# Kernel tuning notes

Measured on AMD Instinct MI355X. Metric: run time of the kernel, lower is better.

Reference implementation:

```python
import jax, jax.numpy as jnp
import numpy as np

NUM_ENT = 100000
NUM_REL = 400
EMB = 100          # emb_dim
OUT = 200          # 2*emb_dim (GCN out channels / ConvE embedding)
E = 500000         # num edges (even: first half 'in', second half 'out')
B = 512            # batch of triples
BN_EPS = 1e-5


def ccorr(a, b):
    # circular correlation: irfft(conj(rfft(a)) * rfft(b))
    fa = jnp.fft.rfft(a, axis=-1)
    fb = jnp.fft.rfft(b, axis=-1)
    return jnp.fft.irfft(jnp.conj(fa) * fb, n=a.shape[-1], axis=-1).astype(a.dtype)


def bn(x, axes):
    # training-mode batchnorm with default affine (gamma=1, beta=0)
    m = jnp.mean(x, axis=axes, keepdims=True)
    v = jnp.var(x, axis=axes, keepdims=True)
    return (x - m) * jax.lax.rsqrt(v + BN_EPS)


def setup_inputs() -> dict:
    key = jax.random.key(0)
    ks = jax.random.split(key, 18)
    s = 0.1
    return {
        'ent_emb': jax.random.normal(ks[0], (NUM_ENT, EMB), jnp.float32) * s,
        'rel_emb': jax.random.normal(ks[1], (NUM_REL, EMB), jnp.float32) * s,
        'in_w': jax.random.normal(ks[2], (EMB, OUT), jnp.float32) * s,
        'out_w': jax.random.normal(ks[3], (EMB, OUT), jnp.float32) * s,
        'loop_w': jax.random.normal(ks[4], (EMB, OUT), jnp.float32) * s,
        'w_rel': jax.random.normal(ks[5], (EMB, OUT), jnp.float32) * s,
        'loop_rel': jax.random.normal(ks[6], (1, EMB), jnp.float32) * s,
        'gcn_bias': jnp.zeros((OUT,), jnp.float32),
        'edge_norm': jax.random.uniform(ks[7], (E,), jnp.float32),
        'conv_w': jax.random.normal(ks[8], (200, 1, 7, 7), jnp.float32) * 0.05,
        'fc_w': jax.random.normal(ks[9], (OUT, 39200), jnp.float32) * 0.01,
        'fc_b': jnp.zeros((OUT,), jnp.float32),
        'b_ent': jnp.zeros((NUM_ENT,), jnp.float32),
        'edge_src': jax.random.randint(ks[10], (E,), 0, NUM_ENT, jnp.int32),
        'edge_dst': jax.random.randint(ks[11], (E,), 0, NUM_ENT, jnp.int32),
        'edge_type': jax.random.randint(ks[12], (E,), 0, NUM_REL, jnp.int32),
        'head': jax.random.randint(ks[13], (B,), 0, NUM_ENT, jnp.int32),
        'rela': jax.random.randint(ks[14], (B,), 0, NUM_REL, jnp.int32),
    }


def reference(ent_emb, rel_emb, in_w, out_w, loop_w, w_rel, loop_rel,
              gcn_bias, edge_norm, conv_w, fc_w, fc_b, b_ent,
              edge_src, edge_dst, edge_type, head, rela):
    # ---- CompGCNCov layer (opn='corr', act=tanh, dropout off / eval) ----
    edge_data = ccorr(ent_emb[edge_src], rel_emb[edge_type])      # [E, EMB]
    half = edge_data.shape[0] // 2
    msg = jnp.concatenate([edge_data[:half] @ in_w,
                           edge_data[half:] @ out_w], axis=0)     # [E, OUT]
    msg = msg * edge_norm[:, None]
    agg = jax.ops.segment_sum(msg, edge_dst, num_segments=ent_emb.shape[0]) / 3.0
    loop = ccorr(ent_emb, jnp.broadcast_to(loop_rel, ent_emb.shape)) @ loop_w / 3.0
    x = agg + loop + gcn_bias
    x = jnp.tanh(bn(x, (0,)))                                     # [NUM_ENT, OUT]
    r = rel_emb @ w_rel                                           # [NUM_REL, OUT]

    # ---- ConvE decoder ----
    h = x[head]                                                   # [B, OUT]
    q = r[rela]                                                   # [B, OUT]
    stack = jnp.concatenate([h[:, None, :], q[:, None, :]], axis=1)
    stack = stack.reshape(-1, 1, 20, 20)                          # [B,1,20,20]
    z = bn(stack, (0, 2, 3))
    z = jax.lax.conv_general_dilated(z, conv_w, (1, 1), 'VALID',
                                     dimension_numbers=('NCHW', 'OIHW', 'NCHW'))
    z = jax.nn.relu(bn(z, (0, 2, 3)))                             # [B,200,14,14]
    z = z.reshape(z.shape[0], -1) @ fc_w.T + fc_b                 # [B, OUT]
    z = jax.nn.relu(bn(z, (0,)))
    score = jax.nn.sigmoid(z @ x.T + b_ent)                       # [B, NUM_ENT]
    return score
```

## Files before the change

### kernel.cpp

```cpp
#include <hip/hip_runtime.h>

#define NENT  100000
#define NREL  400
#define EMB   100
#define NF    51
#define FCMP  102
#define OUTC  200
#define NEDGE 500000
#define HALFE 250000
#define BATCH 512
#define POSN  196
#define FCK   39200
#define BN_EPS 1e-5f
#define CAP   16
#define KSPLIT 175
#define NCOL8  208
#define FCOUT  106496

static constexpr size_t OFF_FA     = 0;
static constexpr size_t OFF_XH     = 0;
static constexpr size_t OFF_ACCIN  = 10200000;
static constexpr size_t OFF_Z1H    = 10200000;
static constexpr size_t OFF_ACCOUT = 20400000;
static constexpr size_t OFF_FCWH   = 20400000;
static constexpr size_t OFF_XBUF   = 30600000;
static constexpr size_t OFF_FB     = 50600000;
static constexpr size_t OFF_FL     = 50640800;
static constexpr size_t OFF_BIGBT  = 50640928;
static constexpr size_t OFF_R      = 50675872;
static constexpr size_t OFF_IMG    = 50755872;
static constexpr size_t OFF_DFTH   = 50755872;
static constexpr size_t OFF_ZH     = 50755872;
static constexpr size_t OFF_DFTC   = 50960672;
static constexpr size_t OFF_DFTS   = 50965772;
static constexpr size_t OFF_Z      = 50970872;
static constexpr size_t OFF_COLSUM = OFF_Z + 102400;
static constexpr size_t OFF_COLSS  = OFF_COLSUM + 200;
static constexpr size_t OFF_BN1    = OFF_COLSS + 200;
static constexpr size_t OFF_CHSUM  = OFF_BN1 + 8;
static constexpr size_t OFF_CHSS   = OFF_CHSUM + 200;
static constexpr size_t WS_END     = OFF_CHSS + 200;

#define NBUCK 200000
static constexpr size_t BK_CNT   = 0;
static constexpr size_t BK_OVFN  = 200000;
static constexpr size_t BK_OVF   = 200004;
static constexpr size_t BK_SLOT  = 700008;

typedef __attribute__((ext_vector_type(8))) _Float16 f16x8;
typedef __attribute__((ext_vector_type(4))) _Float16 f16x4;
typedef __attribute__((ext_vector_type(4))) float f32x4;

__device__ inline unsigned int pkc(float re, float im) {
  union { _Float16 h[2]; unsigned int u; } c;
  c.h[0] = (_Float16)re; c.h[1] = (_Float16)im;
  return c.u;
}
__device__ inline float2 unpk(unsigned int w) {
  union { unsigned int u; _Float16 h[2]; } c; c.u = w;
  return make_float2((float)c.h[0], (float)c.h[1]);
}
__device__ inline float sigf(float v) {
  return __builtin_amdgcn_rcpf(1.0f + __expf(-v));
}

__global__ void k_tables(float* __restrict__ ws) {
  int i = blockIdx.x * 256 + threadIdx.x;
  if (i >= EMB * NF) return;
  int j = i / NF, f = i - j * NF;
  int m = (j * f) % EMB;
  float ang = (float)m * 0.06283185307179586f;
  ws[OFF_DFTC + i] = cosf(ang);
  ws[OFF_DFTS + i] = sinf(ang);
}

__global__ void k_dfth(_Float16* __restrict__ DT) {
  int i = blockIdx.x * 256 + threadIdx.x;
  if (i >= 112 * 128) return;
  int c = i >> 7, k = i & 127;
  float v = 0.f;
  if (c < FCMP && k < EMB) {
    int f = c >> 1;
    int m = (k * f) % EMB;
    float ang = (float)m * 0.06283185307179586f;
    v = (c & 1) ? -sinf(ang) : cosf(ang);
  }
  DT[i] = (_Float16)v;
}

__global__ void __launch_bounds__(256) k_rfft_mfma(const float* __restrict__ A,
                                                   const _Float16* __restrict__ DT,
                                                   _Float16* __restrict__ Fa) {
  int t = threadIdx.x;
  int w = t >> 6, l = t & 63;
  int lr = l & 15, kg = l >> 4;
  size_t row0 = (size_t)blockIdx.x * 128 + w * 32;
  f32x4 acc[2][7];
  #pragma unroll
  for (int i = 0; i < 2; ++i)
    #pragma unroll
    for (int j = 0; j < 7; ++j) acc[i][j] = (f32x4){0.f, 0.f, 0.f, 0.f};

  #pragma unroll
  for (int st = 0; st < 4; ++st) {
    int koff = st * 32 + kg * 8;
    f16x8 a[2];
    #pragma unroll
    for (int i = 0; i < 2; ++i) {
      size_t row = row0 + i * 16 + lr;
      if (row >= NENT) row = NENT - 1;
      f16x8 h;
      if (st < 3) {
        const float* p = A + row * EMB + koff;
        float4 p0 = *(const float4*)p;
        float4 p1 = *(const float4*)(p + 4);
        h[0] = (_Float16)p0.x; h[1] = (_Float16)p0.y; h[2] = (_Float16)p0.z; h[3] = (_Float16)p0.w;
        h[4] = (_Float16)p1.x; h[5] = (_Float16)p1.y; h[6] = (_Float16)p1.z; h[7] = (_Float16)p1.w;
      } else if (kg == 0) {
        float4 p0 = *(const float4*)(A + row * EMB + 96);
        h[0] = (_Float16)p0.x; h[1] = (_Float16)p0.y; h[2] = (_Float16)p0.z; h[3] = (_Float16)p0.w;
        h[4] = (_Float16)0.f; h[5] = (_Float16)0.f; h[6] = (_Float16)0.f; h[7] = (_Float16)0.f;
      } else {
        h = (f16x8)0;
      }
      a[i] = h;
    }
    f16x8 b[7];
    #pragma unroll
    for (int j = 0; j < 7; ++j)
      b[j] = *(const f16x8*)(DT + (size_t)(j * 16 + lr) * 128 + koff);
    #pragma unroll
    for (int i = 0; i < 2; ++i)
      #pragma unroll
      for (int j = 0; j < 7; ++j)
        acc[i][j] = __builtin_amdgcn_mfma_f32_16x16x32_f16(a[i], b[j], acc[i][j], 0, 0, 0);
  }

  #pragma unroll
  for (int i = 0; i < 2; ++i) {
    #pragma unroll
    for (int j = 0; j < 7; ++j) {
      int col = j * 16 + lr;
      if (col < FCMP) {
        #pragma unroll
        for (int r = 0; r < 4; ++r) {
          size_t row = row0 + i * 16 + kg * 4 + r;
          if (row < NENT) Fa[row * FCMP + col] = (_Float16)acc[i][j][r];
        }
      }
    }
  }
}

__global__ void k_rfft(const float* __restrict__ src, unsigned int* __restrict__ dst,
                       const float* __restrict__ dftc, const float* __restrict__ dfts,
                       int nrows) {
  __shared__ float arow[4][EMB];
  int g = threadIdx.x >> 6;
  int lane = threadIdx.x & 63;
  int row = blockIdx.x * 4 + g;
  if (row < nrows) {
    for (int j = lane; j < EMB; j += 64) arow[g][j] = src[(size_t)row * EMB + j];
  }
  __syncthreads();
  if (row < nrows && lane < NF) {
    float re = 0.f, im = 0.f;
    for (int j = 0; j < EMB; ++j) {
      float a = arow[g][j];
      re += a * dftc[j * NF + lane];
      im -= a * dfts[j * NF + lane];
    }
    dst[(size_t)row * NF + lane] = pkc(re, im);
  }
}

__global__ void k_wtilde(const float* __restrict__ in_w, const float* __restrict__ out_w,
                         const float* __restrict__ loop_w, float* __restrict__ ws) {
  int id = blockIdx.x * 256 + threadIdx.x;
  if (id >= NF * OUTC) return;
  int f = id / OUTC, o = id - f * OUTC;
  const float* dftc = ws + OFF_DFTC;
  const float* dfts = ws + OFF_DFTS;
  float ci = 0, si = 0, co = 0, so = 0, cl = 0, sl = 0;
  for (int k = 0; k < EMB; ++k) {
    float c = dftc[k * NF + f], s = dfts[k * NF + f];
    float wi = in_w[k * OUTC + o], wo = out_w[k * OUTC + o], wl = loop_w[k * OUTC + o];
    ci += c * wi; si += s * wi;
    co += c * wo; so += s * wo;
    cl += c * wl; sl += s * wl;
  }
  bool ends = (f == 0) || (f == NF - 1);
  float mult = ends ? 1.0f : 2.0f;
  const float inv3n = 1.0f / (3.0f * (float)EMB);
  _Float16* bt = (_Float16*)(ws + OFF_BIGBT);
  size_t ro = (size_t)o * 336;
  bt[ro + 102 + 2 * f]     = (_Float16)(mult * ci * inv3n);
  bt[ro + 102 + 2 * f + 1] = (_Float16)(ends ? 0.f : (-2.0f * si * inv3n));
  bt[ro + 204 + 2 * f]     = (_Float16)(mult * co * inv3n);
  bt[ro + 204 + 2 * f + 1] = (_Float16)(ends ? 0.f : (-2.0f * so * inv3n));
  float wlre = mult * cl * inv3n;
  float wlim = ends ? 0.f : (-2.0f * sl * inv3n);
  float2 fl = unpk(((const unsigned int*)(ws + OFF_FL))[f]);
  bt[ro + 2 * f]     = (_Float16)(fl.x * wlre + fl.y * wlim);
  bt[ro + 2 * f + 1] = (_Float16)(fl.y * wlre - fl.x * wlim);
}

__global__ void k_bucket(const int* __restrict__ edst, const int* __restrict__ esrc,
                         const int* __restrict__ etyp, const float* __restrict__ enorm,
                         int* __restrict__ cnt, uint2* __restrict__ slot,
                         int* __restrict__ ovfn, int* __restrict__ ovf) {
  int e = blockIdx.x * 256 + threadIdx.x;
  if (e >= NEDGE) return;
  int b = (e < HALFE ? 0 : NENT) + edst[e];
  int pos = atomicAdd(&cnt[b], 1);
  if (pos < CAP) {
    unsigned int p = (unsigned int)esrc[e] | ((unsigned int)etyp[e] << 17);
    slot[(size_t)b * CAP + pos] = make_uint2(p, __float_as_uint(enorm[e]));
  } else {
    int oi = atomicAdd(ovfn, 1);
    if (oi < NEDGE) ovf[oi] = e;
  }
}

__global__ void __launch_bounds__(256) k_agg(const unsigned int* __restrict__ faw,
                                             const unsigned int* __restrict__ fbw,
                                             const int* __restrict__ cnt,
                                             const uint2* __restrict__ slot,
                                             float* __restrict__ accIn, float* __restrict__ accOut) {
  int g = threadIdx.x >> 6;
  int lane = threadIdx.x & 63;
  int d = blockIdx.x * 2 + (g >> 1);
  int sub = g & 1;
  int bucket = sub * NENT + d;
  int n = cnt[bucket];
  if (n > CAP) n = CAP;
  const uint2* sl = slot + (size_t)bucket * CAP;
  uint2 my = make_uint2(0u, 0u);
  if (lane < n) my = sl[lane];
  float ar = 0.f, ai = 0.f;
  for (int i = 0; i < n; i += 4) {
    #pragma unroll
    for (int u = 0; u < 4; ++u) {
      int iu = i + u;
      int ic = (iu < n) ? iu : (n - 1);
      unsigned int p = (unsigned int)__shfl((int)my.x, ic);
      float nor = __uint_as_float((unsigned int)__shfl((int)my.y, ic));
      if (iu >= n) nor = 0.f;
      int s = (int)(p & 0x1FFFFu);
      int ty = (int)(p >> 17);
      if (lane < NF) {
        float2 fa = unpk(faw[(size_t)s * NF + lane]);
        float2 fb = unpk(fbw[(size_t)ty * NF + lane]);
        ar += (fa.x * fb.x + fa.y * fb.y) * nor;
        ai += (fa.x * fb.y - fa.y * fb.x) * nor;
      }
    }
  }
  if (lane < NF) {
    float* dst = sub ? accOut : accIn;
    *(float2*)(dst + (size_t)d * FCMP + 2 * lane) = make_float2(ar, ai);
  }
}

__global__ void k_ovf(const unsigned int* __restrict__ faw, const unsigned int* __restrict__ fbw,
                      const int* __restrict__ esrc, const int* __restrict__ edst,
                      const int* __restrict__ etyp, const float* __restrict__ enorm,
                      const int* __restrict__ ovfn, const int* __restrict__ ovf,
                      float* __restrict__ accIn, float* __restrict__ accOut) {
  int sub = threadIdx.x >> 7;
  int l = threadIdx.x & 127;
  if (l >= FCMP) return;
  int n = *ovfn;
  if (n > NEDGE) n = NEDGE;
  int f = l >> 1, isim = l & 1;
  for (int j = blockIdx.x * 2 + sub; j < n; j += gridDim.x * 2) {
    int e = ovf[j];
    int s = esrc[e], d = edst[e], ty = etyp[e];
    float nor = enorm[e];
    float2 fa = unpk(faw[(size_t)s * NF + f]);
    float2 fb = unpk(fbw[(size_t)ty * NF + f]);
    float v = isim ? (fa.x * fb.y - fa.y * fb.x) : (fa.x * fb.x + fa.y * fb.y);
    float* acc = (e < HALFE) ? accIn : accOut;
    atomicAdd(acc + (size_t)d * FCMP + l, v * nor);
  }
}

__global__ void k_relmat(const float* __restrict__ rel_emb, const float* __restrict__ w_rel,
                         float* __restrict__ r) {
  int id = blockIdx.x * 256 + threadIdx.x;
  if (id >= NREL * OUTC) return;
  int rr = id / OUTC, o = id - rr * OUTC;
  float acc = 0.f;
  for (int k = 0; k < EMB; ++k) acc += rel_emb[rr * EMB + k] * w_rel[k * OUTC + o];
  r[id] = acc;
}

__global__ void __launch_bounds__(256) k_fused_x_mfma(const float* __restrict__ ws,
                                                      _Float16* __restrict__ xpre) {
  int t = threadIdx.x;
  int w = t >> 6, l = t & 63;
  int lr = l & 15, kg = l >> 4;
  size_t row0 = (size_t)blockIdx.x * 128 + w * 32;
  const _Float16* BT = (const _Float16*)(ws + OFF_BIGBT);
  const _Float16* FaH = (const _Float16*)(ws + OFF_FA);
  const float* aI = ws + OFF_ACCIN;
  const float* aO = ws + OFF_ACCOUT;
  f32x4 acc[2][13];
  #pragma unroll
  for (int i = 0; i < 2; ++i)
    #pragma unroll
    for (int j = 0; j < 13; ++j) acc[i][j] = (f32x4){0.f, 0.f, 0.f, 0.f};

  #pragma unroll
  for (int seg = 0; seg < 3; ++seg) {
    #pragma unroll
    for (int st = 0; st < 4; ++st) {
      int koff = st * 32 + kg * 8;
      f16x8 a[2];
      #pragma unroll
      for (int i = 0; i < 2; ++i) {
        size_t row = row0 + i * 16 + lr;
        f16x8 h;
        if (seg == 0) {
          h = *(const f16x8*)(FaH + row * FCMP + koff);
          if (st == 3) {
            #pragma unroll
            for (int e = 0; e < 8; ++e)
              if (koff + e >= FCMP) h[e] = (_Float16)0.f;
          }
        } else {
          const float* p = (seg == 1 ? aI : aO) + row * FCMP + koff;
          float4 p0 = *(const float4*)p;
          float4 p1 = *(const float4*)(p + 4);
          if (st < 3) {
            h[0] = (_Float16)p0.x; h[1] = (_Float16)p0.y; h[2] = (_Float16)p0.z; h[3] = (_Float16)p0.w;
            h[4] = (_Float16)p1.x; h[5] = (_Float16)p1.y; h[6] = (_Float16)p1.z; h[7] = (_Float16)p1.w;
          } else {
            float pv[8] = {p0.x, p0.y, p0.z, p0.w, p1.x, p1.y, p1.z, p1.w};
            #pragma unroll
            for (int e = 0; e < 8; ++e)
              h[e] = (koff + e < FCMP) ? (_Float16)pv[e] : (_Float16)0.f;
          }
        }
        a[i] = h;
      }
      f16x8 b[13];
      #pragma unroll
      for (int j = 0; j < 13; ++j)
        b[j] = *(const f16x8*)(BT + (size_t)(j * 16 + lr) * 336 + seg * FCMP + koff);
      #pragma unroll
      for (int i = 0; i < 2; ++i)
        #pragma unroll
        for (int j = 0; j < 13; ++j)
          acc[i][j] = __builtin_amdgcn_mfma_f32_16x16x32_f16(a[i], b[j], acc[i][j], 0, 0, 0);
    }
  }

  #pragma unroll
  for (int i = 0; i < 2; ++i) {
    #pragma unroll
    for (int j = 0; j < 13; ++j) {
      int col = j * 16 + lr;
      if (col < OUTC) {
        #pragma unroll
        for (int r = 0; r < 4; ++r) {
          size_t row = row0 + i * 16 + kg * 4 + r;
          if (row < NENT) xpre[row * OUTC + col] = (_Float16)acc[i][j][r];
        }
      }
    }
  }
}

__global__ void k_colstats(const _Float16* __restrict__ x, float* __restrict__ colsum,
                           float* __restrict__ colss) {
  int t = threadIdx.x;
  if (t >= OUTC) return;
  size_t r0 = (size_t)blockIdx.x * 500;
  float s1 = 0.f, s2 = 0.f;
  for (int i = 0; i < 500; ++i) {
    float v = (float)x[(r0 + i) * OUTC + t];
    s1 += v; s2 += v * v;
  }
  atomicAdd(colsum + t, s1);
  atomicAdd(colss + t, s2);
}

__global__ void k_bn_tanh(const _Float16* __restrict__ x, _Float16* __restrict__ xh,
                          const float* __restrict__ colsum, const float* __restrict__ colss) {
  size_t i = (size_t)blockIdx.x * 256 + threadIdx.x;
  if (i >= 5000000ull) return;
  f16x4 v = ((const f16x4*)x)[i];
  int c = (int)((i * 4) % OUTC);
  const float inv = 1.0f / (float)NENT;
  float m, q, rs;
  f16x4 h;
  m = colsum[c] * inv;     q = colss[c] * inv - m * m;     rs = rsqrtf(q + BN_EPS); h[0] = (_Float16)tanhf(((float)v[0] - m) * rs);
  m = colsum[c + 1] * inv; q = colss[c + 1] * inv - m * m; rs = rsqrtf(q + BN_EPS); h[1] = (_Float16)tanhf(((float)v[1] - m) * rs);
  m = colsum[c + 2] * inv; q = colss[c + 2] * inv - m * m; rs = rsqrtf(q + BN_EPS); h[2] = (_Float16)tanhf(((float)v[2] - m) * rs);
  m = colsum[c + 3] * inv; q = colss[c + 3] * inv - m * m; rs = rsqrtf(q + BN_EPS); h[3] = (_Float16)tanhf(((float)v[3] - m) * rs);
  *(f16x4*)(xh + i * 4) = h;
}

__global__ void k_fcw_h(const float* __restrict__ w, _Float16* __restrict__ wh) {
  size_t i = (size_t)blockIdx.x * 256 + threadIdx.x;
  if (i >= 980000ull) return;
  float4 v0 = ((const float4*)w)[i * 2];
  float4 v1 = ((const float4*)w)[i * 2 + 1];
  f16x8 h;
  h[0] = (_Float16)v0.x; h[1] = (_Float16)v0.y; h[2] = (_Float16)v0.z; h[3] = (_Float16)v0.w;
  h[4] = (_Float16)v1.x; h[5] = (_Float16)v1.y; h[6] = (_Float16)v1.z; h[7] = (_Float16)v1.w;
  ((f16x8*)wh)[i] = h;
}

__global__ void k_gather_img(const _Float16* __restrict__ xh, const float* __restrict__ r,
                             const int* __restrict__ head, const int* __restrict__ rela,
                             float* __restrict__ img, float* __restrict__ bn1) {
  int b = blockIdx.x, t = threadIdx.x;
  int h = head[b], q = rela[b];
  float s1 = 0.f, s2 = 0.f;
  for (int j = t; j < 400; j += 256) {
    float v = (j < OUTC) ? (float)xh[(size_t)h * OUTC + j] : r[(size_t)q * OUTC + (j - OUTC)];
    img[(size_t)b * 400 + j] = v;
    s1 += v; s2 += v * v;
  }
  for (int off = 32; off; off >>= 1) { s1 += __shfl_down(s1, off); s2 += __shfl_down(s2, off); }
  if ((t & 63) == 0) { atomicAdd(bn1, s1); atomicAdd(bn1 + 1, s2); }
}

__global__ void __launch_bounds__(256) k_conv(const float* __restrict__ img, const float* __restrict__ conv_w,
                                              const float* __restrict__ bn1, _Float16* __restrict__ z1,
                                              float* __restrict__ chsum, float* __restrict__ chss) {
  __shared__ float imgn[400];
  int b = blockIdx.x, t = threadIdx.x;
  float m = bn1[0] * (1.0f / 204800.0f);
  float var = bn1[1] * (1.0f / 204800.0f) - m * m;
  float rs = rsqrtf(var + BN_EPS);
  for (int j = t; j < 400; j += 256) imgn[j] = (img[(size_t)b * 400 + j] - m) * rs;
  __syncthreads();
  if (t < OUTC) {
    float w[49];
    #pragma unroll
    for (int i = 0; i < 49; ++i) w[i] = conv_w[t * 49 + i];
    float s1 = 0.f, s2 = 0.f;
    size_t base = (size_t)b * FCK + (size_t)t * POSN;
    for (int pos = 0; pos < POSN; ++pos) {
      int y = pos / 14, xx = pos - y * 14;
      float acc = 0.f;
      #pragma unroll
      for (int ky = 0; ky < 7; ++ky)
        #pragma unroll
        for (int kx = 0; kx < 7; ++kx)
          acc += imgn[(y + ky) * 20 + xx + kx] * w[ky * 7 + kx];
      z1[base + pos] = (_Float16)acc;
      s1 += acc; s2 += acc * acc;
    }
    atomicAdd(chsum + t, s1);
    atomicAdd(chss + t, s2);
  }
}

__global__ void k_bn2_relu(_Float16* __restrict__ z1, const float* __restrict__ chsum,
                           const float* __restrict__ chss) {
  size_t i = (size_t)blockIdx.x * 256 + threadIdx.x;
  if (i >= 5017600ull) return;
  f16x4 v = ((f16x4*)z1)[i];
  int c = (int)((i * 4 % FCK) / POSN);
  const float inv = 1.0f / (512.0f * 196.0f);
  float m = chsum[c] * inv;
  float var = chss[c] * inv - m * m;
  float rs = rsqrtf(var + BN_EPS);
  #pragma unroll
  for (int e = 0; e < 4; ++e)
    v[e] = (_Float16)fmaxf(((float)v[e] - m) * rs, 0.f);
  ((f16x4*)z1)[i] = v;
}

__global__ void __launch_bounds__(256) k_fc_mfma(const _Float16* __restrict__ A,
                                                 const _Float16* __restrict__ B,
                                                 float* __restrict__ partial) {
  int t = threadIdx.x;
  int w = t >> 6, l = t & 63;
  int lr = l & 15, kg = l >> 4;
  int m0 = blockIdx.y * 128 + w * 32;
  int ks = blockIdx.x;
  f32x4 acc[2][13];
  #pragma unroll
  for (int i = 0; i < 2; ++i)
    #pragma unroll
    for (int j = 0; j < 13; ++j) acc[i][j] = (f32x4){0.f, 0.f, 0.f, 0.f};

  #pragma unroll
  for (int s = 0; s < 7; ++s) {
    int k = (ks * 7 + s) * 32 + kg * 8;
    f16x8 a[2], b[13];
    #pragma unroll
    for (int i = 0; i < 2; ++i)
      a[i] = *(const f16x8*)(A + (size_t)(m0 + i * 16 + lr) * FCK + k);
    #pragma unroll
    for (int j = 0; j < 13; ++j)
      b[j] = *(const f16x8*)(B + (size_t)(j * 16 + lr) * FCK + k);
    #pragma unroll
    for (int i = 0; i < 2; ++i)
      #pragma unroll
      for (int j = 0; j < 13; ++j)
        acc[i][j] = __builtin_amdgcn_mfma_f32_16x16x32_f16(a[i], b[j], acc[i][j], 0, 0, 0);
  }

  float* P = partial + (size_t)ks * FCOUT;
  #pragma unroll
  for (int i = 0; i < 2; ++i) {
    #pragma unroll
    for (int j = 0; j < 13; ++j) {
      int col = j * 16 + lr;
      #pragma unroll
      for (int r = 0; r < 4; ++r) {
        int row = m0 + i * 16 + kg * 4 + r;
        P[(size_t)row * NCOL8 + col] = acc[i][j][r];
      }
    }
  }
}

__global__ void __launch_bounds__(256) k_fc_reduce(const float* __restrict__ partial,
                                                   float* __restrict__ z) {
  int i = blockIdx.x * 256 + threadIdx.x;
  float s = 0.f;
  #pragma unroll 5
  for (int ks = 0; ks < KSPLIT; ++ks)
    s += partial[(size_t)ks * FCOUT + i];
  int row = i / NCOL8, col = i - row * NCOL8;
  if (col < OUTC) z[(size_t)row * OUTC + col] = s;
}

__global__ void k_bn3_relu(const float* __restrict__ z, _Float16* __restrict__ zh) {
  int c = blockIdx.x, lane = threadIdx.x;
  float v[8];
  float s1 = 0.f, s2 = 0.f;
  #pragma unroll
  for (int i = 0; i < 8; ++i) {
    v[i] = z[(size_t)(lane + i * 64) * OUTC + c];
    s1 += v[i]; s2 += v[i] * v[i];
  }
  for (int off = 32; off; off >>= 1) { s1 += __shfl_down(s1, off); s2 += __shfl_down(s2, off); }
  s1 = __shfl(s1, 0); s2 = __shfl(s2, 0);
  float m = s1 * (1.0f / 512.0f);
  float var = s2 * (1.0f / 512.0f) - m * m;
  float rs = rsqrtf(var + BN_EPS);
  #pragma unroll
  for (int i = 0; i < 8; ++i)
    zh[(size_t)(lane + i * 64) * OUTC + c] = (_Float16)fmaxf((v[i] - m) * rs, 0.f);
}

__global__ void __launch_bounds__(256) k_score_mfma(const _Float16* __restrict__ zh,
                                                    const _Float16* __restrict__ xh,
                                                    const float* __restrict__ b_ent,
                                                    float* __restrict__ out) {
  int bid = blockIdx.x;
  int xcd = bid & 7;
  int idx = bid >> 3;
  int bx = (idx >> 2) * 8 + xcd;
  int by = idx & 3;
  if (bx >= 782) return;
  int t = threadIdx.x;
  int w = t >> 6, l = t & 63;
  int lr = l & 15, kg = l >> 4;
  size_t e0 = (size_t)bx * 128 + w * 32;
  int m0 = by * 128;
  f32x4 acc[2][8];
  #pragma unroll
  for (int i = 0; i < 2; ++i)
    #pragma unroll
    for (int j = 0; j < 8; ++j) acc[i][j] = (f32x4){0.f, 0.f, 0.f, 0.f};

  #pragma unroll
  for (int step = 0; step < 7; ++step) {
    int k = step * 32 + kg * 8;
    bool valid = (k < 200);
    f16x8 a[2], b[8];
    #pragma unroll
    for (int i = 0; i < 2; ++i) {
      size_t row = e0 + i * 16 + lr;
      if (row >= NENT) row = NENT - 1;
      a[i] = valid ? *(const f16x8*)(xh + row * OUTC + k) : (f16x8)0;
    }
    #pragma unroll
    for (int j = 0; j < 8; ++j) {
      int mrow = m0 + j * 16 + lr;
      b[j] = valid ? *(const f16x8*)(zh + (size_t)mrow * OUTC + k) : (f16x8)0;
    }
    #pragma unroll
    for (int i = 0; i < 2; ++i)
      #pragma unroll
      for (int j = 0; j < 8; ++j)
        acc[i][j] = __builtin_amdgcn_mfma_f32_16x16x32_f16(a[i], b[j], acc[i][j], 0, 0, 0);
  }

  #pragma unroll
  for (int i = 0; i < 2; ++i) {
    size_t e = e0 + i * 16 + kg * 4;
    if (e < NENT) {
      float4 be = *(const float4*)(b_ent + e);
      #pragma unroll
      for (int j = 0; j < 8; ++j) {
        int m = m0 + j * 16 + lr;
        f32x4 o;
        o[0] = sigf(acc[i][j][0] + be.x);
        o[1] = sigf(acc[i][j][1] + be.y);
        o[2] = sigf(acc[i][j][2] + be.z);
        o[3] = sigf(acc[i][j][3] + be.w);
        __builtin_nontemporal_store(o, (f32x4*)(out + (size_t)m * NENT + e));
      }
    }
  }
}

extern "C" void kernel_launch(void* const* d_in, const int* in_sizes, int n_in,
                              void* d_out, int out_size, void* d_ws, size_t ws_size,
                              hipStream_t stream) {
  (void)in_sizes; (void)n_in; (void)out_size; (void)ws_size;
  const float* ent_emb  = (const float*)d_in[0];
  const float* rel_emb  = (const float*)d_in[1];
  const float* in_w     = (const float*)d_in[2];
  const float* out_w    = (const float*)d_in[3];
  const float* loop_w   = (const float*)d_in[4];
  const float* w_rel    = (const float*)d_in[5];
  const float* loop_rel = (const float*)d_in[6];
  const float* edge_norm= (const float*)d_in[8];
  const float* conv_w   = (const float*)d_in[9];
  const float* fc_w     = (const float*)d_in[10];
  const float* b_ent    = (const float*)d_in[12];
  const int* esrc = (const int*)d_in[13];
  const int* edst = (const int*)d_in[14];
  const int* etyp = (const int*)d_in[15];
  const int* head = (const int*)d_in[16];
  const int* rela = (const int*)d_in[17];
  float* ws  = (float*)d_ws;
  float* out = (float*)d_out;
  int* bk = (int*)(ws + OFF_XBUF);

  (void)hipMemsetAsync(bk + BK_CNT, 0, (size_t)(NBUCK + 1) * 4, stream);
  (void)hipMemsetAsync(ws + OFF_BIGBT, 0, (size_t)34944 * 4, stream);
  (void)hipMemsetAsync(ws + OFF_COLSUM, 0, (WS_END - OFF_COLSUM) * 4, stream);

  k_tables<<<20, 256, 0, stream>>>(ws);
  k_dfth<<<56, 256, 0, stream>>>((_Float16*)(ws + OFF_DFTH));
  k_bucket<<<1954, 256, 0, stream>>>(edst, esrc, etyp, edge_norm,
                                     bk + BK_CNT, (uint2*)(bk + BK_SLOT), bk + BK_OVFN, bk + BK_OVF);
  k_rfft_mfma<<<782, 256, 0, stream>>>(ent_emb, (const _Float16*)(ws + OFF_DFTH),
                                       (_Float16*)(ws + OFF_FA));
  k_rfft<<<100, 256, 0, stream>>>(rel_emb, (unsigned int*)(ws + OFF_FB),
                                  ws + OFF_DFTC, ws + OFF_DFTS, NREL);
  k_rfft<<<1, 256, 0, stream>>>(loop_rel, (unsigned int*)(ws + OFF_FL),
                                ws + OFF_DFTC, ws + OFF_DFTS, 1);
  k_wtilde<<<40, 256, 0, stream>>>(in_w, out_w, loop_w, ws);
  k_agg<<<NENT / 2, 256, 0, stream>>>((const unsigned int*)(ws + OFF_FA),
                                      (const unsigned int*)(ws + OFF_FB),
                                      bk + BK_CNT, (const uint2*)(bk + BK_SLOT),
                                      ws + OFF_ACCIN, ws + OFF_ACCOUT);
  k_ovf<<<64, 256, 0, stream>>>((const unsigned int*)(ws + OFF_FA),
                                (const unsigned int*)(ws + OFF_FB),
                                esrc, edst, etyp, edge_norm,
                                bk + BK_OVFN, bk + BK_OVF, ws + OFF_ACCIN, ws + OFF_ACCOUT);
  k_relmat<<<313, 256, 0, stream>>>(rel_emb, w_rel, ws + OFF_R);
  k_fused_x_mfma<<<782, 256, 0, stream>>>(ws, (_Float16*)(ws + OFF_XBUF));
  k_colstats<<<200, 256, 0, stream>>>((const _Float16*)(ws + OFF_XBUF),
                                      ws + OFF_COLSUM, ws + OFF_COLSS);
  k_bn_tanh<<<19532, 256, 0, stream>>>((const _Float16*)(ws + OFF_XBUF), (_Float16*)(ws + OFF_XH),
                                       ws + OFF_COLSUM, ws + OFF_COLSS);
  k_fcw_h<<<3829, 256, 0, stream>>>(fc_w, (_Float16*)(ws + OFF_FCWH));
  k_gather_img<<<512, 256, 0, stream>>>((const _Float16*)(ws + OFF_XH), ws + OFF_R,
                                        head, rela, ws + OFF_IMG, ws + OFF_BN1);
  k_conv<<<512, 256, 0, stream>>>(ws + OFF_IMG, conv_w, ws + OFF_BN1, (_Float16*)(ws + OFF_Z1H),
                                  ws + OFF_CHSUM, ws + OFF_CHSS);
  k_bn2_relu<<<19600, 256, 0, stream>>>((_Float16*)(ws + OFF_Z1H), ws + OFF_CHSUM, ws + OFF_CHSS);
  k_fc_mfma<<<dim3(KSPLIT, 4), 256, 0, stream>>>((const _Float16*)(ws + OFF_Z1H),
                                                 (const _Float16*)(ws + OFF_FCWH),
                                                 ws + OFF_XBUF);
  k_fc_reduce<<<416, 256, 0, stream>>>(ws + OFF_XBUF, ws + OFF_Z);
  k_bn3_relu<<<200, 64, 0, stream>>>(ws + OFF_Z, (_Float16*)(ws + OFF_ZH));
  k_score_mfma<<<3136, 256, 0, stream>>>((const _Float16*)(ws + OFF_ZH),
                                         (const _Float16*)(ws + OFF_XH),
                                         b_ent, out);
}
```

Before: 693.3 us.

## Switch conv output to position-major layout and transpose FC weights to match

```diff
diff --git a/kernel.cpp b/kernel.cpp
--- a/kernel.cpp
+++ b/kernel.cpp
@@ -402,15 +402,20 @@
   *(f16x4*)(xh + i * 4) = h;
 }
 
-__global__ void k_fcw_h(const float* __restrict__ w, _Float16* __restrict__ wh) {
-  size_t i = (size_t)blockIdx.x * 256 + threadIdx.x;
-  if (i >= 980000ull) return;
-  float4 v0 = ((const float4*)w)[i * 2];
-  float4 v1 = ((const float4*)w)[i * 2 + 1];
-  f16x8 h;
-  h[0] = (_Float16)v0.x; h[1] = (_Float16)v0.y; h[2] = (_Float16)v0.z; h[3] = (_Float16)v0.w;
-  h[4] = (_Float16)v1.x; h[5] = (_Float16)v1.y; h[6] = (_Float16)v1.z; h[7] = (_Float16)v1.w;
-  ((f16x8*)wh)[i] = h;
+__global__ void __launch_bounds__(256) k_fcw_t(const float* __restrict__ w, _Float16* __restrict__ wh) {
+  __shared__ _Float16 tile[50 * 201];
+  int blk = blockIdx.x;
+  int o = blk >> 2, chq = blk & 3;
+  int t = threadIdx.x;
+  for (int j = t; j < 50 * POSN; j += 256) {
+    int ch = j / POSN, pos = j - ch * POSN;
+    tile[ch * 201 + pos] = (_Float16)w[(size_t)o * FCK + (size_t)(chq * 50 + ch) * POSN + pos];
+  }
+  __syncthreads();
+  for (int j = t; j < 50 * POSN; j += 256) {
+    int pos = j / 50, ch = j - pos * 50;
+    wh[(size_t)o * FCK + (size_t)pos * OUTC + chq * 50 + ch] = tile[ch * 201 + pos];
+  }
 }
 
 __global__ void k_gather_img(const _Float16* __restrict__ xh, const float* __restrict__ r,
@@ -432,7 +437,9 @@
                                               const float* __restrict__ bn1, _Float16* __restrict__ z1,
                                               float* __restrict__ chsum, float* __restrict__ chss) {
   __shared__ float imgn[400];
-  int b = blockIdx.x, t = threadIdx.x;
+  int blk = blockIdx.x;
+  int b = blk >> 2, q = blk & 3;
+  int t = threadIdx.x;
   float m = bn1[0] * (1.0f / 204800.0f);
   float var = bn1[1] * (1.0f / 204800.0f) - m * m;
   float rs = rsqrtf(var + BN_EPS);
@@ -443,8 +450,9 @@
     #pragma unroll
     for (int i = 0; i < 49; ++i) w[i] = conv_w[t * 49 + i];
     float s1 = 0.f, s2 = 0.f;
-    size_t base = (size_t)b * FCK + (size_t)t * POSN;
-    for (int pos = 0; pos < POSN; ++pos) {
+    size_t base = (size_t)b * FCK;
+    for (int p = 0; p < 49; ++p) {
+      int pos = q * 49 + p;
       int y = pos / 14, xx = pos - y * 14;
       float acc = 0.f;
       #pragma unroll
@@ -452,7 +460,7 @@
         #pragma unroll
         for (int kx = 0; kx < 7; ++kx)
           acc += imgn[(y + ky) * 20 + xx + kx] * w[ky * 7 + kx];
-      z1[base + pos] = (_Float16)acc;
+      z1[base + (size_t)pos * OUTC + t] = (_Float16)acc;
       s1 += acc; s2 += acc * acc;
     }
     atomicAdd(chsum + t, s1);
@@ -465,14 +473,15 @@
   size_t i = (size_t)blockIdx.x * 256 + threadIdx.x;
   if (i >= 5017600ull) return;
   f16x4 v = ((f16x4*)z1)[i];
-  int c = (int)((i * 4 % FCK) / POSN);
+  int c = (int)((i * 4) % OUTC);
   const float inv = 1.0f / (512.0f * 196.0f);
-  float m = chsum[c] * inv;
-  float var = chss[c] * inv - m * m;
-  float rs = rsqrtf(var + BN_EPS);
-  #pragma unroll
-  for (int e = 0; e < 4; ++e)
+  #pragma unroll
+  for (int e = 0; e < 4; ++e) {
+    float m = chsum[c + e] * inv;
+    float var = chss[c + e] * inv - m * m;
+    float rs = rsqrtf(var + BN_EPS);
     v[e] = (_Float16)fmaxf(((float)v[e] - m) * rs, 0.f);
+  }
   ((f16x4*)z1)[i] = v;
 }
 
@@ -668,11 +677,11 @@
                                       ws + OFF_COLSUM, ws + OFF_COLSS);
   k_bn_tanh<<<19532, 256, 0, stream>>>((const _Float16*)(ws + OFF_XBUF), (_Float16*)(ws + OFF_XH),
                                        ws + OFF_COLSUM, ws + OFF_COLSS);
-  k_fcw_h<<<3829, 256, 0, stream>>>(fc_w, (_Float16*)(ws + OFF_FCWH));
+  k_fcw_t<<<800, 256, 0, stream>>>(fc_w, (_Float16*)(ws + OFF_FCWH));
   k_gather_img<<<512, 256, 0, stream>>>((const _Float16*)(ws + OFF_XH), ws + OFF_R,
                                         head, rela, ws + OFF_IMG, ws + OFF_BN1);
-  k_conv<<<512, 256, 0, stream>>>(ws + OFF_IMG, conv_w, ws + OFF_BN1, (_Float16*)(ws + OFF_Z1H),
-                                  ws + OFF_CHSUM, ws + OFF_CHSS);
+  k_conv<<<2048, 256, 0, stream>>>(ws + OFF_IMG, conv_w, ws + OFF_BN1, (_Float16*)(ws + OFF_Z1H),
+                                   ws + OFF_CHSUM, ws + OFF_CHSS);
   k_bn2_relu<<<19600, 256, 0, stream>>>((_Float16*)(ws + OFF_Z1H), ws + OFF_CHSUM, ws + OFF_CHSS);
   k_fc_mfma<<<dim3(KSPLIT, 4), 256, 0, stream>>>((const _Float16*)(ws + OFF_Z1H),
                                                  (const _Float16*)(ws + OFF_FCWH),
```

New measurement: 702.1 us. Within noise of the previous version (+1.3%).
